# Kernel optimization log

Measured on AMD Instinct MI355X. Metric: run time of the kernel, lower is better.

Reference implementation:

```python
import jax, jax.numpy as jnp
import numpy as np

T, B = 64, 8  # rollout steps x envs; x rows = T*B


def _conv2d(x, w, b=None, pad=1):
    y = jax.lax.conv_general_dilated(x, w, (1, 1), [(pad, pad), (pad, pad)],
                                     dimension_numbers=("NCHW", "OIHW", "NCHW"))
    return y if b is None else y + b[None, :, None, None]


def _maxpool3s2(x):
    return jax.lax.reduce_window(x, -jnp.inf, jax.lax.max, (1, 1, 3, 3), (1, 1, 2, 2),
                                 [(0, 0), (0, 0), (1, 1), (1, 1)])


def _conv_seq(x, cw, cb, rw, rb):
    # Conv -> MaxPool -> ResBlock -> ResBlock
    x = _maxpool3s2(_conv2d(x, cw, cb))
    for i in range(2):
        o = jax.nn.relu(x)
        o = _conv2d(o, rw[2 * i], rb[2 * i])
        o = jax.nn.relu(o)
        o = _conv2d(o, rw[2 * i + 1], rb[2 * i + 1])
        x = o + x
    return x


def _cbam(x, fc1, fc2, spw):
    mlp = lambda v: jax.nn.relu(v @ fc1.T) @ fc2.T
    ca = jax.nn.sigmoid(mlp(x.mean((2, 3))) + mlp(x.max((2, 3))))  # channel attention
    x = x * ca[:, :, None, None]
    sp = jnp.concatenate([x.mean(1, keepdims=True), x.max(1, keepdims=True)], axis=1)
    sa = jax.nn.sigmoid(_conv2d(sp, spw, None, pad=3))  # 7x7 spatial attention
    return x * sa


def setup_inputs():
    key = jax.random.key(0)
    ks = iter(jax.random.split(key, 40))
    f = lambda shape, s=0.05: jax.random.normal(next(ks), shape, jnp.float32) * s
    return {
        "x": f((T * B, 6, 128, 128), 1.0),
        "done": jnp.zeros((T * B,), jnp.float32),
        "gru_state": f((1, B, 128), 1.0),
        "s0_cw": f((16, 6, 3, 3)), "s0_cb": jnp.zeros((16,), jnp.float32),
        "s0_rw": f((4, 16, 16, 3, 3)), "s0_rb": jnp.zeros((4, 16), jnp.float32),
        "s1_cw": f((32, 16, 3, 3)), "s1_cb": jnp.zeros((32,), jnp.float32),
        "s1_rw": f((4, 32, 32, 3, 3)), "s1_rb": jnp.zeros((4, 32), jnp.float32),
        "s2_cw": f((32, 32, 3, 3)), "s2_cb": jnp.zeros((32,), jnp.float32),
        "s2_rw": f((4, 32, 32, 3, 3)), "s2_rb": jnp.zeros((4, 32), jnp.float32),
        "cbam_fc1": f((8, 32)), "cbam_fc2": f((32, 8)), "cbam_spw": f((1, 2, 7, 7)),
        "fc_w": f((256, 8192), 0.01), "fc_b": jnp.zeros((256,), jnp.float32),
        "gru_wih": f((384, 256)), "gru_whh": f((384, 128)),
        "gru_bih": jnp.zeros((384,), jnp.float32), "gru_bhh": jnp.zeros((384,), jnp.float32),
        "actor_w": f((3, 128), 0.01), "actor_b": jnp.zeros((3,), jnp.float32),
        "critic_w": f((1, 128)), "critic_b": jnp.zeros((1,), jnp.float32),
    }


def reference(x, done, gru_state,
              s0_cw, s0_cb, s0_rw, s0_rb,
              s1_cw, s1_cb, s1_rw, s1_rb,
              s2_cw, s2_cb, s2_rw, s2_rb,
              cbam_fc1, cbam_fc2, cbam_spw,
              fc_w, fc_b, gru_wih, gru_whh, gru_bih, gru_bhh,
              actor_w, actor_b, critic_w, critic_b):
    h = _conv_seq(x, s0_cw, s0_cb, s0_rw, s0_rb)  # (TB,16,64,64)
    h = _conv_seq(h, s1_cw, s1_cb, s1_rw, s1_rb)  # (TB,32,32,32)
    h = _conv_seq(h, s2_cw, s2_cb, s2_rw, s2_rb)  # (TB,32,16,16)
    h = jax.nn.relu(h)
    h = _cbam(h, cbam_fc1, cbam_fc2, cbam_spw)
    feat = jax.nn.relu(h.reshape(h.shape[0], -1) @ fc_w.T + fc_b)  # (TB,256)
    seq = feat.reshape(T, B, 256)
    d = done.reshape(T, B)
    h0 = gru_state[0]  # (B,128)

    def step(hprev, xd):
        xt, dt = xd
        hprev = (1.0 - dt)[:, None] * hprev  # done-masking of recurrent state
        gi = xt @ gru_wih.T + gru_bih
        gh = hprev @ gru_whh.T + gru_bhh
        ir, iz, inn = jnp.split(gi, 3, axis=-1)
        hr, hz, hn = jnp.split(gh, 3, axis=-1)
        r = jax.nn.sigmoid(ir + hr)
        z = jax.nn.sigmoid(iz + hz)
        n = jnp.tanh(inn + r * hn)
        hnew = (1.0 - z) * n + z * hprev
        return hnew, hnew

    _, hs = jax.lax.scan(step, h0, (seq, d))  # hs: (T,B,128)
    hidden = hs.reshape(T * B, 128)
    logits = hidden @ actor_w.T + actor_b
    value = hidden @ critic_w.T + critic_b
    return jnp.concatenate([logits, value], axis=-1)  # (TB, n_actions+1)
```

## Files before the change

kernel.cpp:

```cpp
#include <hip/hip_runtime.h>
#include <cstdint>
#include <cfloat>
#include <cmath>

typedef unsigned short ushort_t;
typedef short bf16x8 __attribute__((ext_vector_type(8)));
typedef float f32x4 __attribute__((ext_vector_type(4)));

__device__ inline ushort_t f2bf(float f) {
    union { float f; unsigned u; } v; v.f = f;
    return (ushort_t)((v.u + 0x7fffu + ((v.u >> 16) & 1u)) >> 16);
}
__device__ inline float bf2f(ushort_t u) {
    union { unsigned u; float f; } v; v.u = ((unsigned)u) << 16;
    return v.f;
}
__device__ inline float bflo_f(unsigned w) { union { unsigned u; float f; } v; v.u = w << 16; return v.f; }
__device__ inline float bfhi_f(unsigned w) { union { unsigned u; float f; } v; v.u = w & 0xFFFF0000u; return v.f; }
__device__ inline unsigned pk2(float a, float b) {
    return (unsigned)f2bf(a) | ((unsigned)f2bf(b) << 16);
}
__device__ inline unsigned relu2(unsigned p) {
    unsigned lo = (p & 0x8000u) ? 0u : (p & 0xFFFFu);
    unsigned hi = (p & 0x80000000u) ? 0u : (p & 0xFFFF0000u);
    return lo | hi;
}

struct PPJob { const float* src; ushort_t* dst; int ci; int co; int ci8; };
struct PPArgs { PPJob j[15]; };

__global__ __launch_bounds__(256) void prepack_k(PPArgs a) {
    const PPJob p = a.j[blockIdx.x];
    const int G  = (p.ci8 == 1) ? 1 : (p.ci8 == 2) ? 2 : 3;
    const int cw = p.ci8 * 8;
    const int S  = 4 / p.ci8;
    const int tot = 3 * G * p.co * 32;
    for (int i = threadIdx.x; i < tot; i += 256) {
        const int k = i & 31;
        const int rest = i >> 5;
        const int co = rest % p.co;
        const int rest2 = rest / p.co;
        const int g = rest2 % G;
        const int ky = rest2 / G;
        const int s = k / cw, cio = k % cw;
        const int kx = g * S + s;
        float v = 0.f;
        if (kx < 3 && cio < p.ci) v = p.src[(co * p.ci + cio) * 9 + ky * 3 + kx];
        p.dst[i] = f2bf(v);
    }
}

template<int CIR, int CO, bool NCHWIN>
__global__ __launch_bounds__(256) void convm_k(
    const void* __restrict__ inv, const ushort_t* __restrict__ wp,
    const float* __restrict__ bias, const ushort_t* __restrict__ skip,
    ushort_t* __restrict__ out, int H, int TX, int relu_in)
{
    constexpr int NT  = CO / 16;
    constexpr int CI8 = (CIR + 7) / 8;
    constexpr int G   = (CI8 == 1) ? 1 : (CI8 == 2) ? 2 : 3;
    __shared__ __align__(16) ushort_t in_t[18 * 18 * 40 + 64];

    const int n    = blockIdx.y;
    const int tile = blockIdx.x;
    const int ty0  = (tile / TX) * 16, tx0 = (tile % TX) * 16;
    const int tid  = threadIdx.x;
    const int lane = tid & 63, wv = tid >> 6;
    const int col  = lane & 15, oct = lane >> 4;

    bf16x8 wfrag[3][G][NT];
    #pragma unroll
    for (int ky = 0; ky < 3; ++ky)
        #pragma unroll
        for (int g = 0; g < G; ++g)
            #pragma unroll
            for (int t = 0; t < NT; ++t)
                wfrag[ky][g][t] = *(const bf16x8*)&wp[(((ky * G + g) * CO) + t * 16 + col) * 32 + oct * 8];

    if constexpr (NCHWIN) {
        for (int i = tid; i < 325; i += 256)
            *(uint4*)&in_t[i * 40] = make_uint4(0, 0, 0, 0);
        __syncthreads();
        const float* gin = (const float*)inv;
        constexpr int PR = (CIR + 1) / 2;
        for (int i = tid; i < PR * 324; i += 256) {
            const int px = i % 324, pr = i / 324;
            const int r = px / 18, c = px % 18;
            const int gy = ty0 - 1 + r, gx = tx0 - 1 + c;
            if ((unsigned)gy < (unsigned)H && (unsigned)gx < (unsigned)H) {
                const size_t b0 = (((size_t)n * CIR + pr * 2) * H + gy) * H + gx;
                const float va = gin[b0];
                const float vb = (pr * 2 + 1 < CIR) ? gin[b0 + (size_t)H * H] : 0.f;
                *(unsigned*)&in_t[px * 40 + pr * 2] = pk2(va, vb);
            }
        }
    } else {
        if (tid < 4) *(uint4*)&in_t[324 * 40 + tid * 8] = make_uint4(0, 0, 0, 0);
        const ushort_t* gin = (const ushort_t*)inv;
        for (int i = tid; i < 324 * CI8; i += 256) {
            const int px = i / CI8, oc = i % CI8;
            const int r = px / 18, c = px % 18;
            const int gy = ty0 - 1 + r, gx = tx0 - 1 + c;
            uint4 v = make_uint4(0, 0, 0, 0);
            if ((unsigned)gy < (unsigned)H && (unsigned)gx < (unsigned)H) {
                v = *(const uint4*)&gin[(((size_t)n * H + gy) * H + gx) * CIR + oc * 8];
                if (relu_in) { v.x = relu2(v.x); v.y = relu2(v.y); v.z = relu2(v.z); v.w = relu2(v.w); }
            }
            *(uint4*)&in_t[px * 40 + oc * 8] = v;
        }
    }
    __syncthreads();

    f32x4 acc[4][NT];
    #pragma unroll
    for (int r = 0; r < 4; ++r)
        #pragma unroll
        for (int t = 0; t < NT; ++t)
            acc[r][t] = (f32x4){0.f, 0.f, 0.f, 0.f};

    if constexpr (CI8 <= 2) {
        bf16x8 bv[6][G];
        #pragma unroll
        for (int q = 0; q < 6; ++q) {
            const int iy = wv * 4 + q;
            #pragma unroll
            for (int g = 0; g < G; ++g) {
                int pix, cho;
                if constexpr (CI8 == 1) { pix = col + oct;                 cho = 0; }
                else                    { pix = col + g * 2 + (oct >> 1);  cho = (oct & 1) * 8; }
                bv[q][g] = *(const bf16x8*)&in_t[(iy * 18 + pix) * 40 + cho];
            }
        }
        #pragma unroll
        for (int ky = 0; ky < 3; ++ky)
            #pragma unroll
            for (int r = 0; r < 4; ++r)
                #pragma unroll
                for (int g = 0; g < G; ++g)
                    #pragma unroll
                    for (int t = 0; t < NT; ++t)
                        acc[r][t] = __builtin_amdgcn_mfma_f32_16x16x32_bf16(
                            wfrag[ky][g][t], bv[r + ky][g], acc[r][t], 0, 0, 0);
    } else {
        #pragma unroll
        for (int ky = 0; ky < 3; ++ky)
            #pragma unroll
            for (int r = 0; r < 4; ++r) {
                const int iy = wv * 4 + r + ky;
                #pragma unroll
                for (int g = 0; g < 3; ++g) {
                    const bf16x8 b = *(const bf16x8*)&in_t[(iy * 18 + col + g) * 40 + oct * 8];
                    #pragma unroll
                    for (int t = 0; t < NT; ++t)
                        acc[r][t] = __builtin_amdgcn_mfma_f32_16x16x32_bf16(
                            wfrag[ky][g][t], b, acc[r][t], 0, 0, 0);
                }
            }
    }

    float4 bv4[NT];
    #pragma unroll
    for (int t = 0; t < NT; ++t) bv4[t] = *(const float4*)&bias[t * 16 + oct * 4];
    #pragma unroll
    for (int r = 0; r < 4; ++r) {
        const int gy = ty0 + wv * 4 + r;
        const int gx = tx0 + col;
        const size_t pbase = (((size_t)n * H + gy) * H + gx) * CO + oct * 4;
        #pragma unroll
        for (int t = 0; t < NT; ++t) {
            float v0 = acc[r][t][0] + bv4[t].x;
            float v1 = acc[r][t][1] + bv4[t].y;
            float v2 = acc[r][t][2] + bv4[t].z;
            float v3 = acc[r][t][3] + bv4[t].w;
            if (skip) {
                const uint2 s = *(const uint2*)&skip[pbase + t * 16];
                v0 += bflo_f(s.x); v1 += bfhi_f(s.x);
                v2 += bflo_f(s.y); v3 += bfhi_f(s.y);
            }
            uint2 o;
            o.x = pk2(v0, v1);
            o.y = pk2(v2, v3);
            *(uint2*)&out[pbase + t * 16] = o;
        }
    }
}

__global__ __launch_bounds__(256) void pool_nhwc_k(
    const ushort_t* __restrict__ in, ushort_t* __restrict__ out,
    int NI, int H, int C)
{
    const int HP = H >> 1, C8 = C >> 3;
    const long total = (long)NI * HP * HP * C8;
    long idx = (long)blockIdx.x * 256 + threadIdx.x;
    if (idx >= total) return;
    const int c8 = (int)(idx % C8); long r = idx / C8;
    const int px = (int)(r % HP); r /= HP;
    const int py = (int)(r % HP); const long n = r / HP;
    float m[8];
    #pragma unroll
    for (int k = 0; k < 8; ++k) m[k] = -FLT_MAX;
    for (int dy = 0; dy < 3; ++dy) {
        const int y = 2 * py - 1 + dy;
        if ((unsigned)y >= (unsigned)H) continue;
        for (int dx = 0; dx < 3; ++dx) {
            const int x = 2 * px - 1 + dx;
            if ((unsigned)x >= (unsigned)H) continue;
            const uint4 v = *(const uint4*)&in[(((long)n * H + y) * H + x) * C + c8 * 8];
            m[0] = fmaxf(m[0], bflo_f(v.x)); m[1] = fmaxf(m[1], bfhi_f(v.x));
            m[2] = fmaxf(m[2], bflo_f(v.y)); m[3] = fmaxf(m[3], bfhi_f(v.y));
            m[4] = fmaxf(m[4], bflo_f(v.z)); m[5] = fmaxf(m[5], bfhi_f(v.z));
            m[6] = fmaxf(m[6], bflo_f(v.w)); m[7] = fmaxf(m[7], bfhi_f(v.w));
        }
    }
    uint4 o;
    o.x = (unsigned)f2bf(m[0]) | ((unsigned)f2bf(m[1]) << 16);
    o.y = (unsigned)f2bf(m[2]) | ((unsigned)f2bf(m[3]) << 16);
    o.z = (unsigned)f2bf(m[4]) | ((unsigned)f2bf(m[5]) << 16);
    o.w = (unsigned)f2bf(m[6]) | ((unsigned)f2bf(m[7]) << 16);
    *(uint4*)&out[(((long)n * HP + py) * HP + px) * C + c8 * 8] = o;
}

__global__ __launch_bounds__(256) void gemm_splitk_k(
    const float* __restrict__ A, const float* __restrict__ B,
    float* __restrict__ partial, int M, int N, int K, int KC)
{
    __shared__ __align__(16) float As[32][65];
    __shared__ __align__(16) float Bs[32][65];
    const int m0 = blockIdx.x * 64, n0 = blockIdx.y * 64;
    const int kbase = blockIdx.z * KC;
    const int tid = threadIdx.x;
    const int tx = tid & 15, ty = tid >> 4;

    float acc[4][4];
    #pragma unroll
    for (int i = 0; i < 4; ++i)
        #pragma unroll
        for (int j = 0; j < 4; ++j) acc[i][j] = 0.f;

    for (int k0 = kbase; k0 < kbase + KC; k0 += 32) {
        for (int i = tid; i < 64 * 32; i += 256) {
            const int m = i >> 5, k = i & 31;
            As[k][m] = A[(size_t)(m0 + m) * K + k0 + k];
        }
        for (int i = tid; i < 64 * 32; i += 256) {
            const int nn = i >> 5, k = i & 31;
            Bs[k][nn] = B[(size_t)(n0 + nn) * K + k0 + k];
        }
        __syncthreads();
        #pragma unroll
        for (int k = 0; k < 32; ++k) {
            const float4 a = *(const float4*)&As[k][ty * 4];
            const float4 b = *(const float4*)&Bs[k][tx * 4];
            acc[0][0] = fmaf(a.x, b.x, acc[0][0]);
            acc[0][1] = fmaf(a.x, b.y, acc[0][1]);
            acc[0][2] = fmaf(a.x, b.z, acc[0][2]);
            acc[0][3] = fmaf(a.x, b.w, acc[0][3]);
            acc[1][0] = fmaf(a.y, b.x, acc[1][0]);
            acc[1][1] = fmaf(a.y, b.y, acc[1][1]);
            acc[1][2] = fmaf(a.y, b.z, acc[1][2]);
            acc[1][3] = fmaf(a.y, b.w, acc[1][3]);
            acc[2][0] = fmaf(a.z, b.x, acc[2][0]);
            acc[2][1] = fmaf(a.z, b.y, acc[2][1]);
            acc[2][2] = fmaf(a.z, b.z, acc[2][2]);
            acc[2][3] = fmaf(a.z, b.w, acc[2][3]);
            acc[3][0] = fmaf(a.w, b.x, acc[3][0]);
            acc[3][1] = fmaf(a.w, b.y, acc[3][1]);
            acc[3][2] = fmaf(a.w, b.z, acc[3][2]);
            acc[3][3] = fmaf(a.w, b.w, acc[3][3]);
        }
        __syncthreads();
    }

    float* pbase = partial + (size_t)blockIdx.z * M * N;
    #pragma unroll
    for (int i = 0; i < 4; ++i) {
        float4 o = make_float4(acc[i][0], acc[i][1], acc[i][2], acc[i][3]);
        *(float4*)&pbase[(size_t)(m0 + ty * 4 + i) * N + n0 + tx * 4] = o;
    }
}

__global__ __launch_bounds__(256) void gemm_reduce_k(
    const float* __restrict__ partial, const float* __restrict__ bias,
    float* __restrict__ out, int MN, int N, int S, int relu)
{
    const int idx = blockIdx.x * 256 + threadIdx.x;
    if (idx >= MN) return;
    float s = bias[idx % N];
    for (int i = 0; i < S; ++i) s += partial[(size_t)i * MN + idx];
    if (relu) s = fmaxf(s, 0.f);
    out[idx] = s;
}

__global__ __launch_bounds__(256) void cbam_k(
    const ushort_t* __restrict__ in, const float* __restrict__ fc1,
    const float* __restrict__ fc2, const float* __restrict__ spw,
    float* __restrict__ out)
{
    __shared__ float xl[32][257];
    __shared__ float cmean[32], cmax[32], hidm[8], hidx[8], ca[32];
    __shared__ float spm[256], spx[256], sa[256];
    const int n = blockIdx.x, tid = threadIdx.x;
    const ushort_t* inN = in + (size_t)n * 8192;
    #pragma unroll
    for (int c8 = 0; c8 < 4; ++c8) {
        const uint4 v = *(const uint4*)&inN[tid * 32 + c8 * 8];
        xl[c8 * 8 + 0][tid] = fmaxf(bflo_f(v.x), 0.f);
        xl[c8 * 8 + 1][tid] = fmaxf(bfhi_f(v.x), 0.f);
        xl[c8 * 8 + 2][tid] = fmaxf(bflo_f(v.y), 0.f);
        xl[c8 * 8 + 3][tid] = fmaxf(bfhi_f(v.y), 0.f);
        xl[c8 * 8 + 4][tid] = fmaxf(bflo_f(v.z), 0.f);
        xl[c8 * 8 + 5][tid] = fmaxf(bfhi_f(v.z), 0.f);
        xl[c8 * 8 + 6][tid] = fmaxf(bflo_f(v.w), 0.f);
        xl[c8 * 8 + 7][tid] = fmaxf(bfhi_f(v.w), 0.f);
    }
    __syncthreads();
    if (tid < 32) {
        float s = 0.f, m = -FLT_MAX;
        for (int p = 0; p < 256; ++p) { float v = xl[tid][p]; s += v; m = fmaxf(m, v); }
        cmean[tid] = s * (1.f / 256.f); cmax[tid] = m;
    }
    __syncthreads();
    if (tid < 8) {
        float sm = 0.f, sx = 0.f;
        for (int c = 0; c < 32; ++c) {
            float f = fc1[tid * 32 + c];
            sm += f * cmean[c]; sx += f * cmax[c];
        }
        hidm[tid] = fmaxf(sm, 0.f); hidx[tid] = fmaxf(sx, 0.f);
    }
    __syncthreads();
    if (tid < 32) {
        float s = 0.f;
        for (int h = 0; h < 8; ++h) s += fc2[tid * 8 + h] * (hidm[h] + hidx[h]);
        ca[tid] = 1.f / (1.f + expf(-s));
    }
    __syncthreads();
    {
        float s = 0.f, m = -FLT_MAX;
        for (int c = 0; c < 32; ++c) {
            float v = xl[c][tid] * ca[c];
            xl[c][tid] = v;
            s += v; m = fmaxf(m, v);
        }
        spm[tid] = s * (1.f / 32.f); spx[tid] = m;
    }
    __syncthreads();
    {
        const int y = tid >> 4, x = tid & 15;
        float s = 0.f;
        for (int ky = 0; ky < 7; ++ky) {
            const int yy = y + ky - 3;
            if (yy < 0 || yy >= 16) continue;
            for (int kx = 0; kx < 7; ++kx) {
                const int xx = x + kx - 3;
                if (xx < 0 || xx >= 16) continue;
                const int p = yy * 16 + xx;
                s += spm[p] * spw[ky * 7 + kx] + spx[p] * spw[49 + ky * 7 + kx];
            }
        }
        sa[tid] = 1.f / (1.f + expf(-s));
    }
    __syncthreads();
    float* outN = out + (size_t)n * 8192;
    const float sav = sa[tid];
    for (int c = 0; c < 32; ++c) outN[c * 256 + tid] = xl[c][tid] * sav;
}

__global__ __launch_bounds__(384) void gru_k(
    const float* __restrict__ gi, const float* __restrict__ done,
    const float* __restrict__ h0, const float* __restrict__ whh,
    const float* __restrict__ bhh, float* __restrict__ hidden)
{
    const int b = blockIdx.x, j = threadIdx.x;
    __shared__ __align__(16) float hl[128];
    __shared__ float gh[384];
    float4 wr[32];
    const float4* wrow = (const float4*)(whh + (size_t)j * 128);
    #pragma unroll
    for (int i = 0; i < 32; ++i) wr[i] = wrow[i];
    const float bj = bhh[j];
    if (j < 128) hl[j] = h0[b * 128 + j];
    __syncthreads();
    for (int t = 0; t < 64; ++t) {
        const int rowi = t * 8 + b;
        const float dmask = 1.f - done[rowi];
        if (j < 128) hl[j] *= dmask;
        __syncthreads();
        float s = bj;
        const float4* h4 = (const float4*)hl;
        #pragma unroll
        for (int i = 0; i < 32; ++i) {
            const float4 h = h4[i];
            s = fmaf(wr[i].x, h.x, s);
            s = fmaf(wr[i].y, h.y, s);
            s = fmaf(wr[i].z, h.z, s);
            s = fmaf(wr[i].w, h.w, s);
        }
        gh[j] = s;
        __syncthreads();
        if (j < 128) {
            const float* gir = gi + (size_t)rowi * 384;
            const float r = 1.f / (1.f + expf(-(gir[j] + gh[j])));
            const float z = 1.f / (1.f + expf(-(gir[128 + j] + gh[128 + j])));
            const float nn = tanhf(gir[256 + j] + r * gh[256 + j]);
            const float hm = hl[j];
            const float hn = (1.f - z) * nn + z * hm;
            hl[j] = hn;
            hidden[(size_t)rowi * 128 + j] = hn;
        }
        __syncthreads();
    }
}

__global__ __launch_bounds__(256) void heads_k(
    const float* __restrict__ hidden, const float* __restrict__ aw,
    const float* __restrict__ ab, const float* __restrict__ cw,
    const float* __restrict__ cb, float* __restrict__ out)
{
    const int idx = blockIdx.x * 256 + threadIdx.x;
    const int m = idx >> 2, c = idx & 3;
    const float* h = hidden + (size_t)m * 128;
    const float* w = (c < 3) ? (aw + (size_t)c * 128) : cw;
    float s = (c < 3) ? ab[c] : cb[0];
    for (int k = 0; k < 128; ++k) s = fmaf(h[k], w[k], s);
    out[idx] = s;
}

extern "C" void kernel_launch(void* const* d_in, const int* in_sizes, int n_in,
                              void* d_out, int out_size, void* d_ws, size_t ws_size,
                              hipStream_t stream)
{
    const float* x      = (const float*)d_in[0];
    const float* done   = (const float*)d_in[1];
    const float* gstate = (const float*)d_in[2];
    const float* s0_cw  = (const float*)d_in[3];
    const float* s0_cb  = (const float*)d_in[4];
    const float* s0_rw  = (const float*)d_in[5];
    const float* s0_rb  = (const float*)d_in[6];
    const float* s1_cw  = (const float*)d_in[7];
    const float* s1_cb  = (const float*)d_in[8];
    const float* s1_rw  = (const float*)d_in[9];
    const float* s1_rb  = (const float*)d_in[10];
    const float* s2_cw  = (const float*)d_in[11];
    const float* s2_cb  = (const float*)d_in[12];
    const float* s2_rw  = (const float*)d_in[13];
    const float* s2_rb  = (const float*)d_in[14];
    const float* cfc1   = (const float*)d_in[15];
    const float* cfc2   = (const float*)d_in[16];
    const float* cspw   = (const float*)d_in[17];
    const float* fc_w   = (const float*)d_in[18];
    const float* fc_b   = (const float*)d_in[19];
    const float* gwih   = (const float*)d_in[20];
    const float* gwhh   = (const float*)d_in[21];
    const float* gbih   = (const float*)d_in[22];
    const float* gbhh   = (const float*)d_in[23];
    const float* aw     = (const float*)d_in[24];
    const float* ab     = (const float*)d_in[25];
    const float* cwt    = (const float*)d_in[26];
    const float* cbs    = (const float*)d_in[27];
    float* out = (float*)d_out;

    ushort_t* wsu = (ushort_t*)d_ws;
    ushort_t* SCR = wsu;
    ushort_t* U1  = wsu + 33554432;
    ushort_t* U3  = wsu + 67108864;
    ushort_t* X0  = wsu + 83886080;
    ushort_t* WP  = wsu + 88080384;
    float* CBO   = (float*)SCR;
    float* PART  = (float*)U1;
    float* FEAT  = PART + 4194304;
    float* GI    = FEAT + 131072;
    float* PARTG = GI + 196608;
    float* HID   = PARTG + 786432;

    ushort_t* wp_s0e = WP;
    ushort_t* wp_s0r = WP + 1536;
    ushort_t* wp_s1e = WP + 13824;
    ushort_t* wp_s1r = WP + 19968;
    ushort_t* wp_s2e = WP + 56832;
    ushort_t* wp_s2r = WP + 66048;
    {
        PPArgs a;
        a.j[0] = {s0_cw, wp_s0e, 6, 16, 1};
        for (int i = 0; i < 4; ++i) a.j[1 + i] = {s0_rw + i * 2304, wp_s0r + i * 3072, 16, 16, 2};
        a.j[5] = {s1_cw, wp_s1e, 16, 32, 2};
        for (int i = 0; i < 4; ++i) a.j[6 + i] = {s1_rw + i * 9216, wp_s1r + i * 9216, 32, 32, 4};
        a.j[10] = {s2_cw, wp_s2e, 32, 32, 4};
        for (int i = 0; i < 4; ++i) a.j[11 + i] = {s2_rw + i * 9216, wp_s2r + i * 9216, 32, 32, 4};
        prepack_k<<<15, 256, 0, stream>>>(a);
    }

    for (int c = 0; c < 4; ++c) {
        const float* xin = x + (size_t)c * 128 * 6 * 128 * 128;
        convm_k<6, 16, true><<<dim3(64, 128), 256, 0, stream>>>(
            xin, wp_s0e, s0_cb, nullptr, SCR, 128, 8, 0);
        pool_nhwc_k<<<4096, 256, 0, stream>>>(SCR, U1 + (size_t)c * 8388608, 128, 128, 16);
    }
    convm_k<16, 16, false><<<dim3(16, 512), 256, 0, stream>>>(U1,  wp_s0r + 0 * 3072, s0_rb + 0,  nullptr, SCR, 64, 4, 1);
    convm_k<16, 16, false><<<dim3(16, 512), 256, 0, stream>>>(SCR, wp_s0r + 1 * 3072, s0_rb + 16, U1,      U1,  64, 4, 1);
    convm_k<16, 16, false><<<dim3(16, 512), 256, 0, stream>>>(U1,  wp_s0r + 2 * 3072, s0_rb + 32, nullptr, SCR, 64, 4, 1);
    convm_k<16, 16, false><<<dim3(16, 512), 256, 0, stream>>>(SCR, wp_s0r + 3 * 3072, s0_rb + 48, U1,      U1,  64, 4, 1);
    for (int c = 0; c < 2; ++c) {
        convm_k<16, 32, false><<<dim3(16, 256), 256, 0, stream>>>(
            U1 + (size_t)c * 16777216, wp_s1e, s1_cb, nullptr, SCR, 64, 4, 0);
        pool_nhwc_k<<<4096, 256, 0, stream>>>(SCR, U3 + (size_t)c * 8388608, 256, 64, 32);
    }
    convm_k<32, 32, false><<<dim3(4, 512), 256, 0, stream>>>(U3,  wp_s1r + 0 * 9216, s1_rb + 0,  nullptr, SCR, 32, 2, 1);
    convm_k<32, 32, false><<<dim3(4, 512), 256, 0, stream>>>(SCR, wp_s1r + 1 * 9216, s1_rb + 32, U3,      U3,  32, 2, 1);
    convm_k<32, 32, false><<<dim3(4, 512), 256, 0, stream>>>(U3,  wp_s1r + 2 * 9216, s1_rb + 64, nullptr, SCR, 32, 2, 1);
    convm_k<32, 32, false><<<dim3(4, 512), 256, 0, stream>>>(SCR, wp_s1r + 3 * 9216, s1_rb + 96, U3,      U3,  32, 2, 1);
    convm_k<32, 32, false><<<dim3(4, 512), 256, 0, stream>>>(U3, wp_s2e, s2_cb, nullptr, SCR, 32, 2, 0);
    pool_nhwc_k<<<2048, 256, 0, stream>>>(SCR, X0, 512, 32, 32);
    convm_k<32, 32, false><<<dim3(1, 512), 256, 0, stream>>>(X0,  wp_s2r + 0 * 9216, s2_rb + 0,  nullptr, SCR, 16, 1, 1);
    convm_k<32, 32, false><<<dim3(1, 512), 256, 0, stream>>>(SCR, wp_s2r + 1 * 9216, s2_rb + 32, X0,      X0,  16, 1, 1);
    convm_k<32, 32, false><<<dim3(1, 512), 256, 0, stream>>>(X0,  wp_s2r + 2 * 9216, s2_rb + 64, nullptr, SCR, 16, 1, 1);
    convm_k<32, 32, false><<<dim3(1, 512), 256, 0, stream>>>(SCR, wp_s2r + 3 * 9216, s2_rb + 96, X0,      X0,  16, 1, 1);
    cbam_k<<<512, 256, 0, stream>>>(X0, cfc1, cfc2, cspw, CBO);
    gemm_splitk_k<<<dim3(8, 4, 32), 256, 0, stream>>>(CBO, fc_w, PART, 512, 256, 8192, 256);
    gemm_reduce_k<<<512, 256, 0, stream>>>(PART, fc_b, FEAT, 512 * 256, 256, 32, 1);
    gemm_splitk_k<<<dim3(8, 6, 4), 256, 0, stream>>>(FEAT, gwih, PARTG, 512, 384, 256, 64);
    gemm_reduce_k<<<768, 256, 0, stream>>>(PARTG, gbih, GI, 512 * 384, 384, 4, 0);
    gru_k<<<8, 384, 0, stream>>>(GI, done, gstate, gwhh, gbhh, HID);
    heads_k<<<8, 256, 0, stream>>>(HID, aw, ab, cwt, cbs, out);
}
```

Baseline: 1.143 ms.

## Fuse maxpool into stage entry convolutions using overlapping 14-stride tiles

Adds a POOL template path to the conv kernel. The conv output tile is staged in shared memory and the 3x3 stride-2 max-pool is applied there, writing pooled NHWC directly. Tiles step by 14 pixels so each block holds its pooling halo, which makes some conv work redundant. This drops the separate pool kernels, the full-resolution scratch round trip through global memory, and the chunked launch loops. The GRU step also applies done-masking to the dot product result instead of masking the shared state first, removing one barrier per step.

```diff
diff --git a/kernel.cpp b/kernel.cpp
--- a/kernel.cpp
+++ b/kernel.cpp
@@ -50,7 +50,7 @@
     }
 }
 
-template<int CIR, int CO, bool NCHWIN>
+template<int CIR, int CO, bool NCHWIN, bool POOL>
 __global__ __launch_bounds__(256) void convm_k(
     const void* __restrict__ inv, const ushort_t* __restrict__ wp,
     const float* __restrict__ bias, const ushort_t* __restrict__ skip,
@@ -63,7 +63,13 @@
 
     const int n    = blockIdx.y;
     const int tile = blockIdx.x;
-    const int ty0  = (tile / TX) * 16, tx0 = (tile % TX) * 16;
+    int ty0, tx0;
+    if constexpr (POOL) {
+        ty0 = (tile / TX) * 14; if (ty0 > H - 16) ty0 = H - 16;
+        tx0 = (tile % TX) * 14; if (tx0 > H - 16) tx0 = H - 16;
+    } else {
+        ty0 = (tile / TX) * 16; tx0 = (tile % TX) * 16;
+    }
     const int tid  = threadIdx.x;
     const int lane = tid & 63, wv = tid >> 6;
     const int col  = lane & 15, oct = lane >> 4;
@@ -161,63 +167,83 @@
     float4 bv4[NT];
     #pragma unroll
     for (int t = 0; t < NT; ++t) bv4[t] = *(const float4*)&bias[t * 16 + oct * 4];
-    #pragma unroll
-    for (int r = 0; r < 4; ++r) {
-        const int gy = ty0 + wv * 4 + r;
-        const int gx = tx0 + col;
-        const size_t pbase = (((size_t)n * H + gy) * H + gx) * CO + oct * 4;
-        #pragma unroll
-        for (int t = 0; t < NT; ++t) {
-            float v0 = acc[r][t][0] + bv4[t].x;
-            float v1 = acc[r][t][1] + bv4[t].y;
-            float v2 = acc[r][t][2] + bv4[t].z;
-            float v3 = acc[r][t][3] + bv4[t].w;
-            if (skip) {
-                const uint2 s = *(const uint2*)&skip[pbase + t * 16];
-                v0 += bflo_f(s.x); v1 += bfhi_f(s.x);
-                v2 += bflo_f(s.y); v3 += bfhi_f(s.y);
-            }
-            uint2 o;
-            o.x = pk2(v0, v1);
-            o.y = pk2(v2, v3);
-            *(uint2*)&out[pbase + t * 16] = o;
-        }
-    }
-}
-
-__global__ __launch_bounds__(256) void pool_nhwc_k(
-    const ushort_t* __restrict__ in, ushort_t* __restrict__ out,
-    int NI, int H, int C)
-{
-    const int HP = H >> 1, C8 = C >> 3;
-    const long total = (long)NI * HP * HP * C8;
-    long idx = (long)blockIdx.x * 256 + threadIdx.x;
-    if (idx >= total) return;
-    const int c8 = (int)(idx % C8); long r = idx / C8;
-    const int px = (int)(r % HP); r /= HP;
-    const int py = (int)(r % HP); const long n = r / HP;
-    float m[8];
-    #pragma unroll
-    for (int k = 0; k < 8; ++k) m[k] = -FLT_MAX;
-    for (int dy = 0; dy < 3; ++dy) {
-        const int y = 2 * py - 1 + dy;
-        if ((unsigned)y >= (unsigned)H) continue;
-        for (int dx = 0; dx < 3; ++dx) {
-            const int x = 2 * px - 1 + dx;
-            if ((unsigned)x >= (unsigned)H) continue;
-            const uint4 v = *(const uint4*)&in[(((long)n * H + y) * H + x) * C + c8 * 8];
-            m[0] = fmaxf(m[0], bflo_f(v.x)); m[1] = fmaxf(m[1], bfhi_f(v.x));
-            m[2] = fmaxf(m[2], bflo_f(v.y)); m[3] = fmaxf(m[3], bfhi_f(v.y));
-            m[4] = fmaxf(m[4], bflo_f(v.z)); m[5] = fmaxf(m[5], bfhi_f(v.z));
-            m[6] = fmaxf(m[6], bflo_f(v.w)); m[7] = fmaxf(m[7], bfhi_f(v.w));
-        }
-    }
-    uint4 o;
-    o.x = (unsigned)f2bf(m[0]) | ((unsigned)f2bf(m[1]) << 16);
-    o.y = (unsigned)f2bf(m[2]) | ((unsigned)f2bf(m[3]) << 16);
-    o.z = (unsigned)f2bf(m[4]) | ((unsigned)f2bf(m[5]) << 16);
-    o.w = (unsigned)f2bf(m[6]) | ((unsigned)f2bf(m[7]) << 16);
-    *(uint4*)&out[(((long)n * HP + py) * HP + px) * C + c8 * 8] = o;
+
+    if constexpr (POOL) {
+        __syncthreads();
+        #pragma unroll
+        for (int r = 0; r < 4; ++r) {
+            const int ly = wv * 4 + r;
+            #pragma unroll
+            for (int t = 0; t < NT; ++t) {
+                uint2 o;
+                o.x = pk2(acc[r][t][0] + bv4[t].x, acc[r][t][1] + bv4[t].y);
+                o.y = pk2(acc[r][t][2] + bv4[t].z, acc[r][t][3] + bv4[t].w);
+                *(uint2*)&in_t[(ly * 16 + col) * 40 + t * 16 + oct * 4] = o;
+            }
+        }
+        __syncthreads();
+        const int HP = H >> 1;
+        const int py_lo = (ty0 == 0) ? 0 : (ty0 / 2 + 1);
+        const int px_lo = (tx0 == 0) ? 0 : (tx0 / 2 + 1);
+        const int ny = ty0 / 2 + 7 - py_lo + 1;
+        const int nx = tx0 / 2 + 7 - px_lo + 1;
+        constexpr int C8 = CO / 8;
+        const int items = ny * nx * C8;
+        for (int i = tid; i < items; i += 256) {
+            const int c8 = i % C8; const int rr = i / C8;
+            const int px = px_lo + rr % nx;
+            const int py = py_lo + rr / nx;
+            float m[8];
+            #pragma unroll
+            for (int k = 0; k < 8; ++k) m[k] = -FLT_MAX;
+            #pragma unroll
+            for (int wy = 0; wy < 3; ++wy) {
+                const int gy = 2 * py - 1 + wy;
+                if (gy < 0) continue;
+                const int ly = gy - ty0;
+                #pragma unroll
+                for (int wx = 0; wx < 3; ++wx) {
+                    const int gx = 2 * px - 1 + wx;
+                    if (gx < 0) continue;
+                    const int lx = gx - tx0;
+                    const uint4 v = *(const uint4*)&in_t[(ly * 16 + lx) * 40 + c8 * 8];
+                    m[0] = fmaxf(m[0], bflo_f(v.x)); m[1] = fmaxf(m[1], bfhi_f(v.x));
+                    m[2] = fmaxf(m[2], bflo_f(v.y)); m[3] = fmaxf(m[3], bfhi_f(v.y));
+                    m[4] = fmaxf(m[4], bflo_f(v.z)); m[5] = fmaxf(m[5], bfhi_f(v.z));
+                    m[6] = fmaxf(m[6], bflo_f(v.w)); m[7] = fmaxf(m[7], bfhi_f(v.w));
+                }
+            }
+            uint4 o;
+            o.x = (unsigned)f2bf(m[0]) | ((unsigned)f2bf(m[1]) << 16);
+            o.y = (unsigned)f2bf(m[2]) | ((unsigned)f2bf(m[3]) << 16);
+            o.z = (unsigned)f2bf(m[4]) | ((unsigned)f2bf(m[5]) << 16);
+            o.w = (unsigned)f2bf(m[6]) | ((unsigned)f2bf(m[7]) << 16);
+            *(uint4*)&out[(((size_t)n * HP + py) * HP + px) * CO + c8 * 8] = o;
+        }
+    } else {
+        #pragma unroll
+        for (int r = 0; r < 4; ++r) {
+            const int gy = ty0 + wv * 4 + r;
+            const int gx = tx0 + col;
+            const size_t pbase = (((size_t)n * H + gy) * H + gx) * CO + oct * 4;
+            #pragma unroll
+            for (int t = 0; t < NT; ++t) {
+                float v0 = acc[r][t][0] + bv4[t].x;
+                float v1 = acc[r][t][1] + bv4[t].y;
+                float v2 = acc[r][t][2] + bv4[t].z;
+                float v3 = acc[r][t][3] + bv4[t].w;
+                if (skip) {
+                    const uint2 s = *(const uint2*)&skip[pbase + t * 16];
+                    v0 += bflo_f(s.x); v1 += bfhi_f(s.x);
+                    v2 += bflo_f(s.y); v3 += bfhi_f(s.y);
+                }
+                uint2 o;
+                o.x = pk2(v0, v1);
+                o.y = pk2(v2, v3);
+                *(uint2*)&out[pbase + t * 16] = o;
+            }
+        }
+    }
 }
 
 __global__ __launch_bounds__(256) void gemm_splitk_k(
@@ -384,9 +410,7 @@
     for (int t = 0; t < 64; ++t) {
         const int rowi = t * 8 + b;
         const float dmask = 1.f - done[rowi];
-        if (j < 128) hl[j] *= dmask;
-        __syncthreads();
-        float s = bj;
+        float s = 0.f;
         const float4* h4 = (const float4*)hl;
         #pragma unroll
         for (int i = 0; i < 32; ++i) {
@@ -396,14 +420,14 @@
             s = fmaf(wr[i].z, h.z, s);
             s = fmaf(wr[i].w, h.w, s);
         }
-        gh[j] = s;
+        gh[j] = fmaf(s, dmask, bj);
         __syncthreads();
         if (j < 128) {
             const float* gir = gi + (size_t)rowi * 384;
             const float r = 1.f / (1.f + expf(-(gir[j] + gh[j])));
             const float z = 1.f / (1.f + expf(-(gir[128 + j] + gh[128 + j])));
             const float nn = tanhf(gir[256 + j] + r * gh[256 + j]);
-            const float hm = hl[j];
+            const float hm = hl[j] * dmask;
             const float hn = (1.f - z) * nn + z * hm;
             hl[j] = hn;
             hidden[(size_t)rowi * 128 + j] = hn;
@@ -490,31 +514,24 @@
         prepack_k<<<15, 256, 0, stream>>>(a);
     }
 
-    for (int c = 0; c < 4; ++c) {
-        const float* xin = x + (size_t)c * 128 * 6 * 128 * 128;
-        convm_k<6, 16, true><<<dim3(64, 128), 256, 0, stream>>>(
-            xin, wp_s0e, s0_cb, nullptr, SCR, 128, 8, 0);
-        pool_nhwc_k<<<4096, 256, 0, stream>>>(SCR, U1 + (size_t)c * 8388608, 128, 128, 16);
-    }
-    convm_k<16, 16, false><<<dim3(16, 512), 256, 0, stream>>>(U1,  wp_s0r + 0 * 3072, s0_rb + 0,  nullptr, SCR, 64, 4, 1);
-    convm_k<16, 16, false><<<dim3(16, 512), 256, 0, stream>>>(SCR, wp_s0r + 1 * 3072, s0_rb + 16, U1,      U1,  64, 4, 1);
-    convm_k<16, 16, false><<<dim3(16, 512), 256, 0, stream>>>(U1,  wp_s0r + 2 * 3072, s0_rb + 32, nullptr, SCR, 64, 4, 1);
-    convm_k<16, 16, false><<<dim3(16, 512), 256, 0, stream>>>(SCR, wp_s0r + 3 * 3072, s0_rb + 48, U1,      U1,  64, 4, 1);
-    for (int c = 0; c < 2; ++c) {
-        convm_k<16, 32, false><<<dim3(16, 256), 256, 0, stream>>>(
-            U1 + (size_t)c * 16777216, wp_s1e, s1_cb, nullptr, SCR, 64, 4, 0);
-        pool_nhwc_k<<<4096, 256, 0, stream>>>(SCR, U3 + (size_t)c * 8388608, 256, 64, 32);
-    }
-    convm_k<32, 32, false><<<dim3(4, 512), 256, 0, stream>>>(U3,  wp_s1r + 0 * 9216, s1_rb + 0,  nullptr, SCR, 32, 2, 1);
-    convm_k<32, 32, false><<<dim3(4, 512), 256, 0, stream>>>(SCR, wp_s1r + 1 * 9216, s1_rb + 32, U3,      U3,  32, 2, 1);
-    convm_k<32, 32, false><<<dim3(4, 512), 256, 0, stream>>>(U3,  wp_s1r + 2 * 9216, s1_rb + 64, nullptr, SCR, 32, 2, 1);
-    convm_k<32, 32, false><<<dim3(4, 512), 256, 0, stream>>>(SCR, wp_s1r + 3 * 9216, s1_rb + 96, U3,      U3,  32, 2, 1);
-    convm_k<32, 32, false><<<dim3(4, 512), 256, 0, stream>>>(U3, wp_s2e, s2_cb, nullptr, SCR, 32, 2, 0);
-    pool_nhwc_k<<<2048, 256, 0, stream>>>(SCR, X0, 512, 32, 32);
-    convm_k<32, 32, false><<<dim3(1, 512), 256, 0, stream>>>(X0,  wp_s2r + 0 * 9216, s2_rb + 0,  nullptr, SCR, 16, 1, 1);
-    convm_k<32, 32, false><<<dim3(1, 512), 256, 0, stream>>>(SCR, wp_s2r + 1 * 9216, s2_rb + 32, X0,      X0,  16, 1, 1);
-    convm_k<32, 32, false><<<dim3(1, 512), 256, 0, stream>>>(X0,  wp_s2r + 2 * 9216, s2_rb + 64, nullptr, SCR, 16, 1, 1);
-    convm_k<32, 32, false><<<dim3(1, 512), 256, 0, stream>>>(SCR, wp_s2r + 3 * 9216, s2_rb + 96, X0,      X0,  16, 1, 1);
+    convm_k<6, 16, true, true><<<dim3(81, 512), 256, 0, stream>>>(
+        x, wp_s0e, s0_cb, nullptr, U1, 128, 9, 0);
+    convm_k<16, 16, false, false><<<dim3(16, 512), 256, 0, stream>>>(U1,  wp_s0r + 0 * 3072, s0_rb + 0,  nullptr, SCR, 64, 4, 1);
+    convm_k<16, 16, false, false><<<dim3(16, 512), 256, 0, stream>>>(SCR, wp_s0r + 1 * 3072, s0_rb + 16, U1,      U1,  64, 4, 1);
+    convm_k<16, 16, false, false><<<dim3(16, 512), 256, 0, stream>>>(U1,  wp_s0r + 2 * 3072, s0_rb + 32, nullptr, SCR, 64, 4, 1);
+    convm_k<16, 16, false, false><<<dim3(16, 512), 256, 0, stream>>>(SCR, wp_s0r + 3 * 3072, s0_rb + 48, U1,      U1,  64, 4, 1);
+    convm_k<16, 32, false, true><<<dim3(25, 512), 256, 0, stream>>>(
+        U1, wp_s1e, s1_cb, nullptr, U3, 64, 5, 0);
+    convm_k<32, 32, false, false><<<dim3(4, 512), 256, 0, stream>>>(U3,  wp_s1r + 0 * 9216, s1_rb + 0,  nullptr, SCR, 32, 2, 1);
+    convm_k<32, 32, false, false><<<dim3(4, 512), 256, 0, stream>>>(SCR, wp_s1r + 1 * 9216, s1_rb + 32, U3,      U3,  32, 2, 1);
+    convm_k<32, 32, false, false><<<dim3(4, 512), 256, 0, stream>>>(U3,  wp_s1r + 2 * 9216, s1_rb + 64, nullptr, SCR, 32, 2, 1);
+    convm_k<32, 32, false, false><<<dim3(4, 512), 256, 0, stream>>>(SCR, wp_s1r + 3 * 9216, s1_rb + 96, U3,      U3,  32, 2, 1);
+    convm_k<32, 32, false, true><<<dim3(9, 512), 256, 0, stream>>>(
+        U3, wp_s2e, s2_cb, nullptr, X0, 32, 3, 0);
+    convm_k<32, 32, false, false><<<dim3(1, 512), 256, 0, stream>>>(X0,  wp_s2r + 0 * 9216, s2_rb + 0,  nullptr, SCR, 16, 1, 1);
+    convm_k<32, 32, false, false><<<dim3(1, 512), 256, 0, stream>>>(SCR, wp_s2r + 1 * 9216, s2_rb + 32, X0,      X0,  16, 1, 1);
+    convm_k<32, 32, false, false><<<dim3(1, 512), 256, 0, stream>>>(X0,  wp_s2r + 2 * 9216, s2_rb + 64, nullptr, SCR, 16, 1, 1);
+    convm_k<32, 32, false, false><<<dim3(1, 512), 256, 0, stream>>>(SCR, wp_s2r + 3 * 9216, s2_rb + 96, X0,      X0,  16, 1, 1);
     cbam_k<<<512, 256, 0, stream>>>(X0, cfc1, cfc2, cspw, CBO);
     gemm_splitk_k<<<dim3(8, 4, 32), 256, 0, stream>>>(CBO, fc_w, PART, 512, 256, 8192, 256);
     gemm_reduce_k<<<512, 256, 0, stream>>>(PART, fc_b, FEAT, 512 * 256, 256, 32, 1);
```

After: 1.087 ms. -4.9%, faster.
